# Performance work log

Measured on AMD Instinct MI355X. Metric: run time of the kernel, lower is better.

## Reference

```python
import jax, jax.numpy as jnp
import numpy as np

CUTOFF = 5.0
N_RBF = 20
N_NODES = 16384
N_EDGES = 262144
HID = 128


def setup_inputs() -> dict:
    key = jax.random.key(0)
    ks = jax.random.split(key, 8)
    s = jax.random.normal(ks[0], (N_NODES, HID), dtype=jnp.float32)
    v = jax.random.normal(ks[1], (N_NODES, 3, HID), dtype=jnp.float32)
    r_ij = jax.random.normal(ks[2], (N_EDGES, 3), dtype=jnp.float32)
    edge_src = jax.random.randint(ks[3], (N_EDGES,), 0, N_NODES, dtype=jnp.int32)
    edge_dst = jax.random.randint(ks[4], (N_EDGES,), 0, N_NODES, dtype=jnp.int32)
    W1 = jax.random.normal(ks[5], (HID, HID), dtype=jnp.float32) / np.sqrt(HID)
    b1 = jnp.zeros((HID,), dtype=jnp.float32)
    W2 = jax.random.normal(ks[6], (HID, 3 * HID), dtype=jnp.float32) / np.sqrt(HID)
    b2 = jnp.zeros((3 * HID,), dtype=jnp.float32)
    Wrbf = jax.random.normal(ks[7], (N_RBF, 3 * HID), dtype=jnp.float32) / np.sqrt(N_RBF)
    brbf = jnp.zeros((3 * HID,), dtype=jnp.float32)
    return {"s": s, "v": v, "r_ij": r_ij, "edge_src": edge_src, "edge_dst": edge_dst,
            "W1": W1, "b1": b1, "W2": W2, "b2": b2, "Wrbf": Wrbf, "brbf": brbf}


def reference(s, v, r_ij, edge_src, edge_dst, W1, b1, W2, b2, Wrbf, brbf):
    n_nodes = s.shape[0]
    # distances & unit directions
    d = jnp.linalg.norm(r_ij, axis=-1, keepdims=True)            # [E,1]
    unit = r_ij / d                                              # [E,3]
    # sinc radial basis: sin(n*pi*d/cutoff)/d, n = 1..N_RBF
    n = jnp.arange(1, N_RBF + 1, dtype=s.dtype)
    rbf = jnp.sin(n * jnp.pi * d / CUTOFF) / d                   # [E,20]
    # cosine cutoff
    fcut = 0.5 * (jnp.cos(jnp.pi * d / CUTOFF) + 1.0) * (d < CUTOFF)  # [E,1]
    # scalar filter phi(s): Linear -> SiLU -> Linear, then gather to edges
    phi = jax.nn.silu(s @ W1 + b1) @ W2 + b2                     # [N,384]
    phi_j = phi[edge_src]                                        # [E,384]
    # radial filter, cutoff-weighted
    W = (rbf @ Wrbf + brbf) * fcut                               # [E,384]
    split = phi_j * W                                            # [E,384] hadamard
    x_vv = split[:, :HID]          # gates gathered v_j
    x_s = split[:, HID:2 * HID]    # scalar message
    x_dir = split[:, 2 * HID:]     # gates direction vectors
    # per-edge vector message: v_j * x_vv + unit ⊗ x_dir
    dv_edge = v[edge_src] * x_vv[:, None, :] + unit[:, :, None] * x_dir[:, None, :]  # [E,3,128]
    # scatter-sum to destination nodes
    ds = jax.ops.segment_sum(x_s, edge_dst, num_segments=n_nodes)       # [N,128]
    dv = jax.ops.segment_sum(dv_edge, edge_dst, num_segments=n_nodes)   # [N,3,128]
    return dv, ds
```

## Files before the change

kernel.cpp:

```cpp
#include <hip/hip_runtime.h>
#include <math.h>
#include <stdint.h>

#define N_NODES 16384
#define N_EDGES 262144
#define HID 128
#define NRBF 20
#define CUTOFF 5.0f
#define PI_F 3.14159265358979323846f

#define CSTRIDE 16

typedef __attribute__((ext_vector_type(2))) __fp16 half2_t;
union U32H2 { uint32_t u; half2_t h; float f; };

__device__ inline unsigned short f2bf(float f) {
    unsigned int u = __float_as_uint(f);
    u = u + 0x7FFFu + ((u >> 16) & 1u);
    return (unsigned short)(u >> 16);
}
__device__ inline uint32_t pack2(float lo, float hi) {
    return (uint32_t)f2bf(lo) | ((uint32_t)f2bf(hi) << 16);
}
__device__ inline float blo(uint32_t u) { return __uint_as_float(u << 16); }
__device__ inline float bhi(uint32_t u) { return __uint_as_float(u & 0xFFFF0000u); }
__device__ inline uint32_t pkh2(float a, float b) {
    U32H2 u; u.h = __builtin_amdgcn_cvt_pkrtz(a, b); return u.u;
}

__global__ __launch_bounds__(256) void prep_kernel(
    const float* __restrict__ W1, const float* __restrict__ W2,
    const float* __restrict__ Wrbf,
    int* __restrict__ cnt, uint32_t* __restrict__ W1p,
    uint32_t* __restrict__ W2p, uint32_t* __restrict__ Wrbfp)
{
    const int id = blockIdx.x * 256 + threadIdx.x;
    if (id < 16384) {
        cnt[id] = 0;
    } else if (id < 24576) {
        const int i = id - 16384;
        const int kp = i >> 7, t = i & 127;
        W1p[i] = pkh2(W1[(size_t)(2 * kp) * HID + t],
                      W1[(size_t)(2 * kp + 1) * HID + t]);
    } else if (id < 49152) {
        const int i = id - 24576;
        const int kp = i / 384, rem = i % 384;
        W2p[i] = pkh2(W2[(size_t)(2 * kp) * 384 + rem],
                      W2[(size_t)(2 * kp + 1) * 384 + rem]);
    } else if (id < 49152 + 3840) {
        const int i = id - 49152;
        const int j = i / 384, rem = i % 384;
        Wrbfp[i] = pkh2(Wrbf[(size_t)(2 * j) * 384 + rem],
                        Wrbf[(size_t)(2 * j + 1) * 384 + rem]);
    }
}

#define PB 32
__global__ __launch_bounds__(512, 4) void phi_kernel(
    const float* __restrict__ s, const float* __restrict__ v,
    const uint32_t* __restrict__ W1p, const float* __restrict__ b1,
    const uint32_t* __restrict__ W2p, const float* __restrict__ b2,
    const int* __restrict__ edst, int* __restrict__ cnt,
    uint2* __restrict__ guv, uint32_t* __restrict__ gw)
{
    const int tid = threadIdx.x;
    const int ch  = tid & 127;
    const int sub = tid >> 7;
    const int node0 = blockIdx.x * PB;

    atomicAdd(&cnt[edst[blockIdx.x * 512 + tid]], 1);

    __shared__ uint32_t sL2[PB][64];
    __shared__ float    hL[PB][HID];
    __shared__ uint32_t hL2[PB][64];

    #pragma unroll
    for (int q = 0; q < 4; ++q) {
        const int idx = q * 512 + tid;
        const int i = idx >> 6, c = idx & 63;
        const float2 sv = *(const float2*)&s[(size_t)(node0 + i) * HID + 2 * c];
        sL2[i][c] = pkh2(sv.x, sv.y);
    }
    __syncthreads();

    float h[8];
    const float bb1 = b1[ch];
    #pragma unroll
    for (int i = 0; i < 8; ++i) h[i] = bb1;

    for (int kp = 0; kp < 64; kp += 2) {
        U32H2 wa; wa.u = W1p[kp * 128 + ch];
        U32H2 wb; wb.u = W1p[(kp + 1) * 128 + ch];
        #pragma unroll
        for (int i = 0; i < 8; ++i) {
            U32H2 ca; ca.u = sL2[sub * 8 + i][kp];
            U32H2 cb; cb.u = sL2[sub * 8 + i][kp + 1];
            h[i] = __builtin_amdgcn_fdot2(ca.h, wa.h, h[i], false);
            h[i] = __builtin_amdgcn_fdot2(cb.h, wb.h, h[i], false);
        }
    }
    #pragma unroll
    for (int i = 0; i < 8; ++i) {
        const float x = h[i];
        hL[sub * 8 + i][ch] = x / (1.0f + expf(-x));
    }
    __syncthreads();
    #pragma unroll
    for (int q = 0; q < 4; ++q) {
        const int idx = q * 512 + tid;
        const int i = idx >> 6, c = idx & 63;
        hL2[i][c] = pkh2(hL[i][2 * c], hL[i][2 * c + 1]);
    }
    __syncthreads();

    float a0[8], a1[8], a2[8];
    #pragma unroll
    for (int i = 0; i < 8; ++i) { a0[i] = 0.f; a1[i] = 0.f; a2[i] = 0.f; }

    for (int kp = 0; kp < 64; ++kp) {
        U32H2 wA; wA.u = W2p[(kp * 3 + 0) * 128 + ch];
        U32H2 wB; wB.u = W2p[(kp * 3 + 1) * 128 + ch];
        U32H2 wC; wC.u = W2p[(kp * 3 + 2) * 128 + ch];
        #pragma unroll
        for (int i = 0; i < 8; ++i) {
            U32H2 hh; hh.u = hL2[sub * 8 + i][kp];
            a0[i] = __builtin_amdgcn_fdot2(hh.h, wA.h, a0[i], false);
            a1[i] = __builtin_amdgcn_fdot2(hh.h, wB.h, a1[i], false);
            a2[i] = __builtin_amdgcn_fdot2(hh.h, wC.h, a2[i], false);
        }
    }
    const float bb2a = b2[ch], bb2b = b2[128 + ch], bb2c = b2[256 + ch];
    #pragma unroll
    for (int i = 0; i < 8; ++i) {
        const int node = node0 + sub * 8 + i;
        const size_t nrow = (size_t)node * 384;
        const float p0 = a0[i] + bb2a;
        const float p1 = a1[i] + bb2b;
        const float p2 = a2[i] + bb2c;
        const float v0 = v[nrow + ch];
        const float v1 = v[nrow + 128 + ch];
        const float v2 = v[nrow + 256 + ch];
        const size_t gi = (size_t)node * HID + ch;
        guv[gi] = make_uint2(pack2(p0, p1), pack2(p2, v0));
        gw[gi]  = pack2(v1, v2);
    }
}

__global__ __launch_bounds__(256) void scan_kernel(const int* __restrict__ cnt,
                                                   int* __restrict__ row_ptr,
                                                   int* __restrict__ cur)
{
    __shared__ int part[256];
    const int tid = threadIdx.x;
    const int4* c4 = (const int4*)cnt;

    int4 loc[16];
    int s = 0;
    #pragma unroll
    for (int j = 0; j < 16; ++j) {
        loc[j] = c4[tid * 16 + j];
        s += loc[j].x + loc[j].y + loc[j].z + loc[j].w;
    }
    part[tid] = s;
    __syncthreads();
    #pragma unroll
    for (int d = 1; d < 256; d <<= 1) {
        const int add = (tid >= d) ? part[tid - d] : 0;
        __syncthreads();
        part[tid] += add;
        __syncthreads();
    }
    int off = (tid == 0) ? 0 : part[tid - 1];
    const int base = tid * 64;
    #pragma unroll
    for (int j = 0; j < 16; ++j) {
        const int4 q = loc[j];
        row_ptr[base + j*4 + 0] = off; cur[base + j*4 + 0] = off; off += q.x;
        row_ptr[base + j*4 + 1] = off; cur[base + j*4 + 1] = off; off += q.y;
        row_ptr[base + j*4 + 2] = off; cur[base + j*4 + 2] = off; off += q.z;
        row_ptr[base + j*4 + 3] = off; cur[base + j*4 + 3] = off; off += q.w;
    }
    if (tid == 255) row_ptr[16384] = off;
}

__global__ __launch_bounds__(256) void scatter_kernel(
    const float* __restrict__ r_ij, const int* __restrict__ esrc,
    const int* __restrict__ edst, int* __restrict__ cur,
    int* __restrict__ soff, uint32_t* __restrict__ coef)
{
    const int e = blockIdx.x * 256 + threadIdx.x;
    if (e >= N_EDGES) return;
    const float rx = r_ij[(size_t)e * 3 + 0];
    const float ry = r_ij[(size_t)e * 3 + 1];
    const float rz = r_ij[(size_t)e * 3 + 2];
    const float d = sqrtf(rx * rx + ry * ry + rz * rz);
    const float inv_d = 1.0f / d;
    float sx, cx;
    sincosf((PI_F / CUTOFF) * d, &sx, &cx);
    const float fcut = (d < CUTOFF) ? 0.5f * (cx + 1.0f) : 0.0f;

    float cf[NRBF];
    const float gfac = inv_d * fcut;
    const float twocx = 2.0f * cx;
    float sm1 = sx, sm2 = 0.0f;
    cf[0] = sx * gfac;
    #pragma unroll
    for (int n = 1; n < NRBF; ++n) {
        const float sn = twocx * sm1 - sm2;
        sm2 = sm1; sm1 = sn;
        cf[n] = sn * gfac;
    }

    uint32_t cp[10];
    #pragma unroll
    for (int j = 0; j < 10; ++j) cp[j] = pkh2(cf[2 * j], cf[2 * j + 1]);

    const int pos = atomicAdd(&cur[edst[e]], 1);
    soff[pos] = esrc[e] * 128;
    uint4* c4 = (uint4*)(coef + (size_t)pos * CSTRIDE);
    c4[0] = make_uint4(__float_as_uint(rx * inv_d), __float_as_uint(ry * inv_d),
                       __float_as_uint(rz * inv_d), __float_as_uint(fcut));
    c4[1] = make_uint4(cp[0], cp[1], cp[2], cp[3]);
    c4[2] = make_uint4(cp[4], cp[5], cp[6], cp[7]);
    c4[3] = make_uint4(cp[8], cp[9], 0u, 0u);
}

__global__ __launch_bounds__(256, 6) void gather_kernel(
    const uint2* __restrict__ guv, const uint32_t* __restrict__ gw,
    const int* __restrict__ soff, const uint32_t* __restrict__ coef,
    const int* __restrict__ row_ptr, const uint32_t* __restrict__ Wrbfp,
    const float* __restrict__ brbf,
    float* __restrict__ dv, float* __restrict__ ds)
{
    const int ch   = threadIdx.x & 127;
    const int node = blockIdx.x * 2 + (threadIdx.x >> 7);

    uint32_t wq0[10], wq1[10], wq2[10];
    #pragma unroll
    for (int j = 0; j < 10; ++j) {
        wq0[j] = Wrbfp[(j * 3 + 0) * 128 + ch];
        wq1[j] = Wrbfp[(j * 3 + 1) * 128 + ch];
        wq2[j] = Wrbfp[(j * 3 + 2) * 128 + ch];
    }
    #pragma unroll
    for (int j = 0; j < 10; ++j) {
        asm volatile("" : "+v"(wq0[j]), "+v"(wq1[j]), "+v"(wq2[j]));
    }
    const float br0 = brbf[ch], br1 = brbf[128 + ch], br2 = brbf[256 + ch];

    const int beg = row_ptr[node];
    const int end = row_ptr[node + 1];
    const int nb  = (end - beg) >> 2;

    float a0 = 0.f, a1 = 0.f, a2 = 0.f, as = 0.f;

    uint2 A2[4], B2[4];
    uint32_t Aw[4], Bw[4];

#define LOADB(P2, Pw, bi) do {                                                \
    const int iu_ = __builtin_amdgcn_readfirstlane(beg + (bi) * 4);           \
    const int* sp_ = soff + iu_;                                              \
    const int o0 = sp_[0] + ch, o1 = sp_[1] + ch,                             \
              o2 = sp_[2] + ch, o3 = sp_[3] + ch;                             \
    P2[0] = guv[o0]; P2[1] = guv[o1]; P2[2] = guv[o2]; P2[3] = guv[o3];       \
    Pw[0] = gw[o0];  Pw[1] = gw[o1];  Pw[2] = gw[o2];  Pw[3] = gw[o3];        \
    const uint32_t* cq_ = coef + (size_t)iu_ * CSTRIDE;                       \
    const uint32_t t0_ = cq_[0],  t1_ = cq_[16],                              \
                   t2_ = cq_[32], t3_ = cq_[48];                              \
    asm volatile("" :: "s"(t0_), "s"(t1_), "s"(t2_), "s"(t3_));               \
} while (0)

#define CONSUME(P2, Pw, bi) do {                                              \
    const uint32_t* cp_ = coef +                                              \
        (size_t)__builtin_amdgcn_readfirstlane(beg + (bi) * 4) * CSTRIDE;     \
    _Pragma("unroll")                                                         \
    for (int k = 0; k < 4; ++k) {                                             \
        const float ux = __uint_as_float(cp_[k * CSTRIDE + 0]);               \
        const float uy = __uint_as_float(cp_[k * CSTRIDE + 1]);               \
        const float uz = __uint_as_float(cp_[k * CSTRIDE + 2]);               \
        const float fc = __uint_as_float(cp_[k * CSTRIDE + 3]);               \
        float W0 = fc * br0;                                                  \
        float W1 = fc * br1;                                                  \
        float W2 = fc * br2;                                                  \
        _Pragma("unroll")                                                     \
        for (int j = 0; j < 10; ++j) {                                        \
            U32H2 cc; cc.u = cp_[k * CSTRIDE + 4 + j];                        \
            U32H2 w0_; w0_.u = wq0[j];                                        \
            U32H2 w1_; w1_.u = wq1[j];                                        \
            U32H2 w2_; w2_.u = wq2[j];                                        \
            W0 = __builtin_amdgcn_fdot2(cc.h, w0_.h, W0, false);              \
            W1 = __builtin_amdgcn_fdot2(cc.h, w1_.h, W1, false);              \
            W2 = __builtin_amdgcn_fdot2(cc.h, w2_.h, W2, false);              \
        }                                                                     \
        const uint32_t p0 = P2[k].x, p1 = P2[k].y, p2 = Pw[k];                \
        const float xv = blo(p0) * W0;                                        \
        const float xs = bhi(p0) * W1;                                        \
        const float xd = blo(p1) * W2;                                        \
        a0 += bhi(p1) * xv + ux * xd;                                         \
        a1 += blo(p2) * xv + uy * xd;                                         \
        a2 += bhi(p2) * xv + uz * xd;                                         \
        as += xs;                                                             \
    }                                                                         \
} while (0)

    if (nb > 0) {
        const int last = nb - 1;
        LOADB(A2, Aw, 0);
        LOADB(B2, Bw, (1 < last ? 1 : last));
        int b = 0;
        for (; b + 2 < nb; b += 2) {
            CONSUME(A2, Aw, b);
            LOADB(A2, Aw, b + 2);
            CONSUME(B2, Bw, b + 1);
            LOADB(B2, Bw, (b + 3 < last ? b + 3 : last));
        }
        const int rem = nb - b;
        CONSUME(A2, Aw, b);
        if (rem == 2) CONSUME(B2, Bw, b + 1);
    }

    for (int i = beg + (nb << 2); i < end; ++i) {
        const int iu = __builtin_amdgcn_readfirstlane(i);
        const int o = soff[iu] + ch;
        const uint2 P = guv[o];
        const uint32_t p2 = gw[o];
        const uint32_t* cp = coef + (size_t)iu * CSTRIDE;
        const float ux = __uint_as_float(cp[0]);
        const float uy = __uint_as_float(cp[1]);
        const float uz = __uint_as_float(cp[2]);
        const float fc = __uint_as_float(cp[3]);
        float W0 = fc * br0;
        float W1 = fc * br1;
        float W2 = fc * br2;
        #pragma unroll
        for (int j = 0; j < 10; ++j) {
            U32H2 cc; cc.u = cp[4 + j];
            U32H2 w0_; w0_.u = wq0[j];
            U32H2 w1_; w1_.u = wq1[j];
            U32H2 w2_; w2_.u = wq2[j];
            W0 = __builtin_amdgcn_fdot2(cc.h, w0_.h, W0, false);
            W1 = __builtin_amdgcn_fdot2(cc.h, w1_.h, W1, false);
            W2 = __builtin_amdgcn_fdot2(cc.h, w2_.h, W2, false);
        }
        const uint32_t p0 = P.x, p1 = P.y;
        const float xv = blo(p0) * W0;
        const float xs = bhi(p0) * W1;
        const float xd = blo(p1) * W2;
        a0 += bhi(p1) * xv + ux * xd;
        a1 += blo(p2) * xv + uy * xd;
        a2 += bhi(p2) * xv + uz * xd;
        as += xs;
    }

#undef LOADB
#undef CONSUME

    const size_t orow = (size_t)node * 384;
    dv[orow + ch]       = a0;
    dv[orow + 128 + ch] = a1;
    dv[orow + 256 + ch] = a2;
    ds[(size_t)node * HID + ch] = as;
}

extern "C" void kernel_launch(void* const* d_in, const int* in_sizes, int n_in,
                              void* d_out, int out_size, void* d_ws, size_t ws_size,
                              hipStream_t stream)
{
    const float* s    = (const float*)d_in[0];
    const float* v    = (const float*)d_in[1];
    const float* r_ij = (const float*)d_in[2];
    const int*   esrc = (const int*)d_in[3];
    const int*   edst = (const int*)d_in[4];
    const float* W1   = (const float*)d_in[5];
    const float* b1   = (const float*)d_in[6];
    const float* W2   = (const float*)d_in[7];
    const float* b2   = (const float*)d_in[8];
    const float* Wrbf = (const float*)d_in[9];
    const float* brbf = (const float*)d_in[10];

    float* out = (float*)d_out;
    float* dv  = out;
    float* ds  = out + (size_t)N_NODES * 3 * HID;

    char* ws = (char*)d_ws;
    uint2*    guv     = (uint2*)   (ws + 0);
    uint32_t* gw      = (uint32_t*)(ws + 16777216);
    uint32_t* coef    = (uint32_t*)(ws + 25165824);
    int*      soff    = (int*)     (ws + 41943040);
    int*      cnt     = (int*)     (ws + 42991616);
    int*      row_ptr = (int*)     (ws + 43057152);
    int*      cur     = (int*)     (ws + 43122816);
    uint32_t* W1p     = (uint32_t*)(ws + 43188352);
    uint32_t* W2p     = (uint32_t*)(ws + 43221120);
    uint32_t* Wrbfp   = (uint32_t*)(ws + 43319424);

    prep_kernel<<<208, 256, 0, stream>>>(W1, W2, Wrbf, cnt, W1p, W2p, Wrbfp);
    phi_kernel<<<N_NODES / PB, 512, 0, stream>>>(s, v, W1p, b1, W2p, b2,
                                                 edst, cnt, guv, gw);
    scan_kernel<<<1, 256, 0, stream>>>(cnt, row_ptr, cur);
    scatter_kernel<<<N_EDGES / 256, 256, 0, stream>>>(r_ij, esrc, edst, cur,
                                                      soff, coef);
    gather_kernel<<<N_NODES / 2, 256, 0, stream>>>(guv, gw, soff, coef, row_ptr,
                                                   Wrbfp, brbf, dv, ds);
}
```

Baseline: 140.9 us.

## Move edge counting into prep kernel and fuse edge scatter into phi kernel

Edge-degree counting moves out of the phi kernel into the weight-packing prep kernel, and the count array is now zeroed with a memset. The scan runs before phi, so the per-edge scatter work (RBF coefficients, CSR slot atomics) can be folded into the phi kernel. This cuts one launch and lets the scatter's memory traffic overlap the phi GEMM compute. The cost is an extra memset call and more register pressure in the fused kernel, and the fused kernel now has to wait for the single-block scan.

After: 136.6 us. -3.0%, faster.

```diff
diff --git a/kernel.cpp b/kernel.cpp
--- a/kernel.cpp
+++ b/kernel.cpp
@@ -30,37 +30,75 @@
 
 __global__ __launch_bounds__(256) void prep_kernel(
     const float* __restrict__ W1, const float* __restrict__ W2,
-    const float* __restrict__ Wrbf,
+    const float* __restrict__ Wrbf, const int* __restrict__ edst,
     int* __restrict__ cnt, uint32_t* __restrict__ W1p,
     uint32_t* __restrict__ W2p, uint32_t* __restrict__ Wrbfp)
 {
     const int id = blockIdx.x * 256 + threadIdx.x;
-    if (id < 16384) {
-        cnt[id] = 0;
-    } else if (id < 24576) {
-        const int i = id - 16384;
-        const int kp = i >> 7, t = i & 127;
-        W1p[i] = pkh2(W1[(size_t)(2 * kp) * HID + t],
-                      W1[(size_t)(2 * kp + 1) * HID + t]);
-    } else if (id < 49152) {
-        const int i = id - 24576;
+    if (id < 8192) {
+        const int kp = id >> 7, t = id & 127;
+        W1p[id] = pkh2(W1[(size_t)(2 * kp) * HID + t],
+                       W1[(size_t)(2 * kp + 1) * HID + t]);
+    } else if (id < 32768) {
+        const int i = id - 8192;
         const int kp = i / 384, rem = i % 384;
         W2p[i] = pkh2(W2[(size_t)(2 * kp) * 384 + rem],
                       W2[(size_t)(2 * kp + 1) * 384 + rem]);
-    } else if (id < 49152 + 3840) {
-        const int i = id - 49152;
+    } else if (id < 36608) {
+        const int i = id - 32768;
         const int j = i / 384, rem = i % 384;
         Wrbfp[i] = pkh2(Wrbf[(size_t)(2 * j) * 384 + rem],
                         Wrbf[(size_t)(2 * j + 1) * 384 + rem]);
-    }
+    } else if (id < 36608 + N_EDGES) {
+        atomicAdd(&cnt[edst[id - 36608]], 1);
+    }
+}
+
+__global__ __launch_bounds__(256) void scan_kernel(const int* __restrict__ cnt,
+                                                   int* __restrict__ row_ptr,
+                                                   int* __restrict__ cur)
+{
+    __shared__ int part[256];
+    const int tid = threadIdx.x;
+    const int4* c4 = (const int4*)cnt;
+
+    int4 loc[16];
+    int s = 0;
+    #pragma unroll
+    for (int j = 0; j < 16; ++j) {
+        loc[j] = c4[tid * 16 + j];
+        s += loc[j].x + loc[j].y + loc[j].z + loc[j].w;
+    }
+    part[tid] = s;
+    __syncthreads();
+    #pragma unroll
+    for (int d = 1; d < 256; d <<= 1) {
+        const int add = (tid >= d) ? part[tid - d] : 0;
+        __syncthreads();
+        part[tid] += add;
+        __syncthreads();
+    }
+    int off = (tid == 0) ? 0 : part[tid - 1];
+    const int base = tid * 64;
+    #pragma unroll
+    for (int j = 0; j < 16; ++j) {
+        const int4 q = loc[j];
+        row_ptr[base + j*4 + 0] = off; cur[base + j*4 + 0] = off; off += q.x;
+        row_ptr[base + j*4 + 1] = off; cur[base + j*4 + 1] = off; off += q.y;
+        row_ptr[base + j*4 + 2] = off; cur[base + j*4 + 2] = off; off += q.z;
+        row_ptr[base + j*4 + 3] = off; cur[base + j*4 + 3] = off; off += q.w;
+    }
+    if (tid == 255) row_ptr[16384] = off;
 }
 
 #define PB 32
-__global__ __launch_bounds__(512, 4) void phi_kernel(
+__global__ __launch_bounds__(512, 4) void phi_scatter_kernel(
     const float* __restrict__ s, const float* __restrict__ v,
     const uint32_t* __restrict__ W1p, const float* __restrict__ b1,
     const uint32_t* __restrict__ W2p, const float* __restrict__ b2,
-    const int* __restrict__ edst, int* __restrict__ cnt,
+    const float* __restrict__ r_ij, const int* __restrict__ esrc,
+    const int* __restrict__ edst, int* __restrict__ cur,
+    int* __restrict__ soff, uint32_t* __restrict__ coef,
     uint2* __restrict__ guv, uint32_t* __restrict__ gw)
 {
     const int tid = threadIdx.x;
@@ -68,7 +106,44 @@
     const int sub = tid >> 7;
     const int node0 = blockIdx.x * PB;
 
-    atomicAdd(&cnt[edst[blockIdx.x * 512 + tid]], 1);
+    {
+        const int e = blockIdx.x * 512 + tid;
+        const float rx = r_ij[(size_t)e * 3 + 0];
+        const float ry = r_ij[(size_t)e * 3 + 1];
+        const float rz = r_ij[(size_t)e * 3 + 2];
+        const float d = sqrtf(rx * rx + ry * ry + rz * rz);
+        const float inv_d = 1.0f / d;
+        float sx, cx;
+        sincosf((PI_F / CUTOFF) * d, &sx, &cx);
+        const float fcut = (d < CUTOFF) ? 0.5f * (cx + 1.0f) : 0.0f;
+
+        float cf[NRBF];
+        const float gfac = inv_d * fcut;
+        const float twocx = 2.0f * cx;
+        float sm1 = sx, sm2 = 0.0f;
+        cf[0] = sx * gfac;
+        #pragma unroll
+        for (int n = 1; n < NRBF; ++n) {
+            const float sn = twocx * sm1 - sm2;
+            sm2 = sm1; sm1 = sn;
+            cf[n] = sn * gfac;
+        }
+
+        uint32_t cp[10];
+        #pragma unroll
+        for (int j = 0; j < 10; ++j) cp[j] = pkh2(cf[2 * j], cf[2 * j + 1]);
+
+        const int pos = atomicAdd(&cur[edst[e]], 1);
+        soff[pos] = esrc[e] * 128;
+        uint4* c4 = (uint4*)(coef + (size_t)pos * CSTRIDE);
+        c4[0] = make_uint4(__float_as_uint(rx * inv_d),
+                           __float_as_uint(ry * inv_d),
+                           __float_as_uint(rz * inv_d),
+                           __float_as_uint(fcut));
+        c4[1] = make_uint4(cp[0], cp[1], cp[2], cp[3]);
+        c4[2] = make_uint4(cp[4], cp[5], cp[6], cp[7]);
+        c4[3] = make_uint4(cp[8], cp[9], 0u, 0u);
+    }
 
     __shared__ uint32_t sL2[PB][64];
     __shared__ float    hL[PB][HID];
@@ -144,85 +219,6 @@
         guv[gi] = make_uint2(pack2(p0, p1), pack2(p2, v0));
         gw[gi]  = pack2(v1, v2);
     }
-}
-
-__global__ __launch_bounds__(256) void scan_kernel(const int* __restrict__ cnt,
-                                                   int* __restrict__ row_ptr,
-                                                   int* __restrict__ cur)
-{
-    __shared__ int part[256];
-    const int tid = threadIdx.x;
-    const int4* c4 = (const int4*)cnt;
-
-    int4 loc[16];
-    int s = 0;
-    #pragma unroll
-    for (int j = 0; j < 16; ++j) {
-        loc[j] = c4[tid * 16 + j];
-        s += loc[j].x + loc[j].y + loc[j].z + loc[j].w;
-    }
-    part[tid] = s;
-    __syncthreads();
-    #pragma unroll
-    for (int d = 1; d < 256; d <<= 1) {
-        const int add = (tid >= d) ? part[tid - d] : 0;
-        __syncthreads();
-        part[tid] += add;
-        __syncthreads();
-    }
-    int off = (tid == 0) ? 0 : part[tid - 1];
-    const int base = tid * 64;
-    #pragma unroll
-    for (int j = 0; j < 16; ++j) {
-        const int4 q = loc[j];
-        row_ptr[base + j*4 + 0] = off; cur[base + j*4 + 0] = off; off += q.x;
-        row_ptr[base + j*4 + 1] = off; cur[base + j*4 + 1] = off; off += q.y;
-        row_ptr[base + j*4 + 2] = off; cur[base + j*4 + 2] = off; off += q.z;
-        row_ptr[base + j*4 + 3] = off; cur[base + j*4 + 3] = off; off += q.w;
-    }
-    if (tid == 255) row_ptr[16384] = off;
-}
-
-__global__ __launch_bounds__(256) void scatter_kernel(
-    const float* __restrict__ r_ij, const int* __restrict__ esrc,
-    const int* __restrict__ edst, int* __restrict__ cur,
-    int* __restrict__ soff, uint32_t* __restrict__ coef)
-{
-    const int e = blockIdx.x * 256 + threadIdx.x;
-    if (e >= N_EDGES) return;
-    const float rx = r_ij[(size_t)e * 3 + 0];
-    const float ry = r_ij[(size_t)e * 3 + 1];
-    const float rz = r_ij[(size_t)e * 3 + 2];
-    const float d = sqrtf(rx * rx + ry * ry + rz * rz);
-    const float inv_d = 1.0f / d;
-    float sx, cx;
-    sincosf((PI_F / CUTOFF) * d, &sx, &cx);
-    const float fcut = (d < CUTOFF) ? 0.5f * (cx + 1.0f) : 0.0f;
-
-    float cf[NRBF];
-    const float gfac = inv_d * fcut;
-    const float twocx = 2.0f * cx;
-    float sm1 = sx, sm2 = 0.0f;
-    cf[0] = sx * gfac;
-    #pragma unroll
-    for (int n = 1; n < NRBF; ++n) {
-        const float sn = twocx * sm1 - sm2;
-        sm2 = sm1; sm1 = sn;
-        cf[n] = sn * gfac;
-    }
-
-    uint32_t cp[10];
-    #pragma unroll
-    for (int j = 0; j < 10; ++j) cp[j] = pkh2(cf[2 * j], cf[2 * j + 1]);
-
-    const int pos = atomicAdd(&cur[edst[e]], 1);
-    soff[pos] = esrc[e] * 128;
-    uint4* c4 = (uint4*)(coef + (size_t)pos * CSTRIDE);
-    c4[0] = make_uint4(__float_as_uint(rx * inv_d), __float_as_uint(ry * inv_d),
-                       __float_as_uint(rz * inv_d), __float_as_uint(fcut));
-    c4[1] = make_uint4(cp[0], cp[1], cp[2], cp[3]);
-    c4[2] = make_uint4(cp[4], cp[5], cp[6], cp[7]);
-    c4[3] = make_uint4(cp[8], cp[9], 0u, 0u);
 }
 
 __global__ __launch_bounds__(256, 6) void gather_kernel(
@@ -394,12 +390,14 @@
     uint32_t* W2p     = (uint32_t*)(ws + 43221120);
     uint32_t* Wrbfp   = (uint32_t*)(ws + 43319424);
 
-    prep_kernel<<<208, 256, 0, stream>>>(W1, W2, Wrbf, cnt, W1p, W2p, Wrbfp);
-    phi_kernel<<<N_NODES / PB, 512, 0, stream>>>(s, v, W1p, b1, W2p, b2,
-                                                 edst, cnt, guv, gw);
+    hipMemsetAsync(cnt, 0, 16384 * sizeof(int), stream);
+
+    prep_kernel<<<1167, 256, 0, stream>>>(W1, W2, Wrbf, edst, cnt,
+                                          W1p, W2p, Wrbfp);
     scan_kernel<<<1, 256, 0, stream>>>(cnt, row_ptr, cur);
-    scatter_kernel<<<N_EDGES / 256, 256, 0, stream>>>(r_ij, esrc, edst, cur,
-                                                      soff, coef);
+    phi_scatter_kernel<<<512, 512, 0, stream>>>(s, v, W1p, b1, W2p, b2,
+                                                r_ij, esrc, edst, cur,
+                                                soff, coef, guv, gw);
     gather_kernel<<<N_NODES / 2, 256, 0, stream>>>(guv, gw, soff, coef, row_ptr,
                                                    Wrbfp, brbf, dv, ds);
 }
```
